# Optimization experiments

Hardware: AMD Instinct MI355X
Metric: run time of the kernel (lower is better)

Reference implementation:

```python
import jax, jax.numpy as jnp
import numpy as np

B, N, E, H = 2, 2048, 2048, 16
D = E // H  # head_dim = 128


def setup_inputs() -> dict:
    key = jax.random.key(0)
    k1, k2, k3, k4 = jax.random.split(key, 4)
    x = jax.random.normal(k1, (B, N, E), dtype=jnp.float32)
    Wq = jax.random.normal(k2, (E, E), dtype=jnp.float32) * 0.02
    Wkv = jax.random.normal(k3, (2 * E, E), dtype=jnp.float32) * 0.02
    Wout = jax.random.normal(k4, (E, E), dtype=jnp.float32) * 0.02
    return {"x": x, "Wq": Wq, "Wkv": Wkv, "Wout": Wout}


def reference(x, Wq, Wkv, Wout):
    # projections (torch Linear: y = x @ W.T)
    q = x @ Wq.T                      # [b, n, e]
    kv = x @ Wkv.T                    # [b, n, 2e]
    k, v = jnp.split(kv, 2, axis=-1)  # each [b, n, e]

    def split_heads(t):
        return t.reshape(B, N, H, D).transpose(0, 2, 1, 3)  # [b, h, n, d]

    q, k, v = split_heads(q), split_heads(k), split_heads(v)

    scale = D ** -0.5
    sim = jnp.einsum('bhid,bhjd->bhij', q * scale, k)  # [b, h, n, n]

    # causal mask: triu(j - i + 1) masks strictly-future positions
    mask_value = -jnp.finfo(sim.dtype).max
    causal_mask = jnp.triu(jnp.ones((N, N), dtype=bool), k=1)
    sim = jnp.where(causal_mask, mask_value, sim)

    attn = jax.nn.softmax(sim, axis=-1)
    out = jnp.einsum('bhij,bhjd->bhid', attn, v)  # [b, h, n, d]
    out = out.transpose(0, 2, 1, 3).reshape(B, N, E)
    return out @ Wout.T
```

## Files before the change

### kernel.cpp

```cpp
#include <hip/hip_runtime.h>


typedef __bf16 bf16;
typedef bf16 bf16x2 __attribute__((ext_vector_type(2)));
typedef bf16 bf16x4 __attribute__((ext_vector_type(4)));
typedef bf16 bf16x8 __attribute__((ext_vector_type(8)));
typedef float f32x4 __attribute__((ext_vector_type(4)));
typedef float f32x16 __attribute__((ext_vector_type(16)));

typedef const __attribute__((address_space(1))) void cg_void;
typedef __attribute__((address_space(3))) void lds_void;

#define MFMA16(a, b, c) __builtin_amdgcn_mfma_f32_16x16x32_bf16((a), (b), (c), 0, 0, 0)
#define MFMA32(a, b, c) __builtin_amdgcn_mfma_f32_32x32x16_bf16((a), (b), (c), 0, 0, 0)

__device__ __forceinline__ void async_load16(const bf16* g, bf16* l) {
  __builtin_amdgcn_global_load_lds((cg_void*)g, (lds_void*)l, 16, 0, 0);
}

__global__ __launch_bounds__(256) void cast_all_kernel(
    const float* __restrict__ x, const float* __restrict__ wq,
    const float* __restrict__ wkv, const float* __restrict__ wout,
    bf16* __restrict__ xb, bf16* __restrict__ wqkvb, bf16* __restrict__ woutb) {
  long i = (long)blockIdx.x * 256 + threadIdx.x;
  const float* src; bf16* dst; long off;
  if (i < 1048576)      { src = x;    dst = xb;            off = i; }
  else if (i < 2621440) { src = wq;   dst = wqkvb;         off = i - 1048576;
                          if (off >= 524288) { src = wkv; dst = wqkvb + 4194304; off -= 524288; } }
  else                  { src = wout; dst = woutb;         off = i - 2621440; }
  float4 f0 = ((const float4*)src)[2 * off];
  float4 f1 = ((const float4*)src)[2 * off + 1];
  bf16x8 o;
  o[0] = (bf16)f0.x; o[1] = (bf16)f0.y; o[2] = (bf16)f0.z; o[3] = (bf16)f0.w;
  o[4] = (bf16)f1.x; o[5] = (bf16)f1.y; o[6] = (bf16)f1.z; o[7] = (bf16)f1.w;
  ((bf16x8*)dst)[off] = o;
}

template <typename OutT>
__global__ __launch_bounds__(256, 4)
void gemm_bt_kernel(const bf16* __restrict__ A, const bf16* __restrict__ B,
                    OutT* __restrict__ C, int K, int NN) {
  __shared__ __attribute__((aligned(16))) bf16 As[128 * 32];
  __shared__ __attribute__((aligned(16))) bf16 Bs[128 * 32];
  const int tid = threadIdx.x;
  const int wave = tid >> 6, lane = tid & 63;
  const int quad = lane >> 4, l15 = lane & 15;
  const int m0 = blockIdx.y * 128, n0 = blockIdx.x * 128;
  const int wm = (wave >> 1) * 64, wn = (wave & 1) * 64;

  f32x4 acc[4][4];
#pragma unroll
  for (int i = 0; i < 4; ++i)
#pragma unroll
    for (int j = 0; j < 4; ++j) acc[i][j] = {0.f, 0.f, 0.f, 0.f};

  const int srow = tid >> 2;
  const int scol = (tid & 3) * 8;
  const bf16* aG = A + (size_t)(m0 + srow) * K + scol;
  const bf16* bG = B + (size_t)(n0 + srow) * K + scol;
  bf16* aL = As + srow * 32 + scol;
  bf16* bL = Bs + srow * 32 + scol;
  const size_t gstep = (size_t)64 * K;

  for (int kt = 0; kt < K; kt += 32) {
    __syncthreads();
    async_load16(aG, aL);
    async_load16(aG + gstep, aL + 64 * 32);
    async_load16(bG, bL);
    async_load16(bG + gstep, bL + 64 * 32);
    aG += 32; bG += 32;
    __syncthreads();

    bf16x8 af[4], bfr[4];
#pragma unroll
    for (int i = 0; i < 4; ++i)
      af[i] = *(const bf16x8*)(As + (wm + i * 16 + l15) * 32 + quad * 8);
#pragma unroll
    for (int j = 0; j < 4; ++j)
      bfr[j] = *(const bf16x8*)(Bs + (wn + j * 16 + l15) * 32 + quad * 8);
#pragma unroll
    for (int i = 0; i < 4; ++i)
#pragma unroll
      for (int j = 0; j < 4; ++j) acc[i][j] = MFMA16(af[i], bfr[j], acc[i][j]);
  }

#pragma unroll
  for (int i = 0; i < 4; ++i) {
#pragma unroll
    for (int r = 0; r < 4; ++r) {
      int row = m0 + wm + i * 16 + quad * 4 + r;
      size_t base = (size_t)row * NN + n0 + wn + l15;
#pragma unroll
      for (int j = 0; j < 4; ++j) C[base + j * 16] = (OutT)acc[i][j][r];
    }
  }
}

__global__ __launch_bounds__(256) void vtrans_kernel(const bf16* __restrict__ qkvb,
                                                     bf16* __restrict__ vt) {
  constexpr int QKV = 6144, NSEQ = 2048, E = 2048;
  __shared__ __attribute__((aligned(16))) bf16 Ts[64 * 64];
  const int t = threadIdx.x;
  const int n0 = blockIdx.x * 64, f0 = blockIdx.y * 64, bb = blockIdx.z;
#pragma unroll
  for (int p = 0; p < 2; ++p) {
    int c = p * 256 + t;
    int i = c >> 3, jc = c & 7;
    bf16x8 v = *(const bf16x8*)(qkvb + (size_t)(bb * NSEQ + n0 + i) * QKV + 4096 + f0 + jc * 8);
    *(bf16x8*)(Ts + i * 64 + ((jc + i) & 7) * 8) = v;
  }
  __syncthreads();
#pragma unroll
  for (int p = 0; p < 2; ++p) {
    int c = p * 256 + t;
    int fl = c >> 3, nl = (c & 7) * 8;
    bf16x8 o;
#pragma unroll
    for (int k = 0; k < 8; ++k) {
      int row = nl + k;
      o[k] = Ts[row * 64 + (((fl >> 3) + row) & 7) * 8 + (fl & 7)];
    }
    *(bf16x8*)(vt + (size_t)(bb * E + f0 + fl) * NSEQ + n0 + nl) = o;
  }
}

__global__ __launch_bounds__(256, 2)
void attn_kernel(const bf16* __restrict__ qkv, const bf16* __restrict__ vt,
                 bf16* __restrict__ yb) {
  constexpr int NSEQ = 2048, E = 2048, QKV = 6144;
  __shared__ __attribute__((aligned(16))) bf16 Ks[2][64 * 128];
  __shared__ __attribute__((aligned(16))) bf16 Vs[2][128 * 64];
  const int tid = threadIdx.x;
  const int wave = tid >> 6, lane = tid & 63;
  const int l31 = lane & 31, half = lane >> 5;
  const int id = blockIdx.x;
  const int slot = (id >> 3) & 15;
  const int bh = (id & 7) | ((id >> 7) << 3);
  const int b = bh >> 4, h = bh & 15;
  const int qt = (slot < 8) ? slot : 23 - slot;
  const float c1 = 0.08838834764831845f * 1.44269504088896f;

  const int krow_s = tid >> 4, kch_s = tid & 15;
  const int vrow_s = tid >> 3, vch_s = tid & 7;
  const bf16* kg = qkv + (size_t)(b * NSEQ) * QKV + 2048 + h * 128;
  const bf16* vg = vt + (size_t)b * E * NSEQ + (size_t)(h * 128) * NSEQ;

  const int diag = 2 * qt + (wave >> 1);
  const int ktmax = 2 * qt + 1;

  {
    bf16* kdst = Ks[0] + tid * 8;
    bf16* vdst = Vs[0] + tid * 8;
#pragma unroll
    for (int p = 0; p < 4; ++p) {
      int r = p * 16 + krow_s;
      async_load16(kg + (size_t)r * QKV + (kch_s ^ (r & 7)) * 8, kdst + p * 2048);
    }
#pragma unroll
    for (int p = 0; p < 4; ++p) {
      int r = p * 32 + vrow_s;
      async_load16(vg + (size_t)r * NSEQ + (vch_s ^ (r & 7)) * 8, vdst + p * 2048);
    }
  }

  const int qrow = qt * 128 + wave * 32 + l31;
  bf16x8 qf[8];
  {
    const bf16* qp = qkv + (size_t)(b * NSEQ + qrow) * QKV + h * 128 + half * 8;
#pragma unroll
    for (int k8 = 0; k8 < 8; ++k8) qf[k8] = *(const bf16x8*)(qp + k8 * 16);
  }

  float m = -3.0e38f, l = 0.f;
  f32x16 accO[4];
#pragma unroll
  for (int md = 0; md < 4; ++md)
#pragma unroll
    for (int r = 0; r < 16; ++r) accO[md][r] = 0.f;

  union PU { unsigned u; bf16x2 h; };
  union FU { bf16x8 v; unsigned u[4]; };

  for (int kt = 0; kt <= ktmax; ++kt) {
    const int cur = kt & 1;
    __syncthreads();

    if (kt < ktmax) {
      const int nxt = kt + 1;
      bf16* kdst = Ks[1 - cur] + tid * 8;
      bf16* vdst = Vs[1 - cur] + tid * 8;
#pragma unroll
      for (int p = 0; p < 4; ++p) {
        int r = p * 16 + krow_s;
        async_load16(kg + (size_t)(nxt * 64 + r) * QKV + (kch_s ^ (r & 7)) * 8, kdst + p * 2048);
      }
#pragma unroll
      for (int p = 0; p < 4; ++p) {
        int r = p * 32 + vrow_s;
        async_load16(vg + (size_t)r * NSEQ + nxt * 64 + (vch_s ^ (r & 7)) * 8, vdst + p * 2048);
      }
    }

    if (kt > diag) continue;

    const bf16* ks = Ks[cur];
    const bf16* vs = Vs[cur];

    f32x16 st[2];
#pragma unroll
    for (int mt = 0; mt < 2; ++mt)
#pragma unroll
      for (int r = 0; r < 16; ++r) st[mt][r] = 0.f;
#pragma unroll
    for (int k8 = 0; k8 < 8; ++k8) {
#pragma unroll
      for (int mt = 0; mt < 2; ++mt) {
        int row = mt * 32 + l31;
        int sl = (k8 * 2 + half) ^ (row & 7);
        bf16x8 kf = *(const bf16x8*)(ks + row * 128 + sl * 8);
        st[mt] = MFMA32(kf, qf[k8], st[mt]);
      }
    }

    if (kt == diag) {
#pragma unroll
      for (int mt = 0; mt < 2; ++mt)
#pragma unroll
        for (int r = 0; r < 16; ++r) {
          int t = kt * 64 + mt * 32 + (r & 3) + 8 * (r >> 2) + 4 * half;
          if (t > qrow) st[mt][r] = -3.0e38f;
        }
    }

    float mx = -3.0e38f;
#pragma unroll
    for (int mt = 0; mt < 2; ++mt)
#pragma unroll
      for (int r = 0; r < 16; ++r) mx = fmaxf(mx, st[mt][r]);
    mx = fmaxf(mx, __shfl_xor(mx, 32));
    float mnew = fmaxf(m, mx);
    float alpha = exp2f((m - mnew) * c1);
    float mc = mnew * c1;
    m = mnew;

    float psum = 0.f;
    unsigned pown[2][4][2];
#pragma unroll
    for (int mt = 0; mt < 2; ++mt)
#pragma unroll
      for (int qd = 0; qd < 4; ++qd)
#pragma unroll
        for (int pr = 0; pr < 2; ++pr) {
          float p0 = exp2f(st[mt][qd * 4 + pr * 2] * c1 - mc);
          float p1 = exp2f(st[mt][qd * 4 + pr * 2 + 1] * c1 - mc);
          psum += p0 + p1;
          PU a; a.h[0] = (bf16)p0; a.h[1] = (bf16)p1;
          pown[mt][qd][pr] = a.u;
        }
    psum += __shfl_xor(psum, 32);
    l = l * alpha + psum;

#pragma unroll
    for (int md = 0; md < 4; ++md)
#pragma unroll
      for (int r = 0; r < 16; ++r) accO[md][r] *= alpha;

#pragma unroll
    for (int mt = 0; mt < 2; ++mt)
#pragma unroll
      for (int c = 0; c < 2; ++c) {
        const int qa = 2 * c, qb = 2 * c + 1;
        unsigned ra0 = __shfl_xor(pown[mt][qa][0], 32);
        unsigned ra1 = __shfl_xor(pown[mt][qa][1], 32);
        unsigned rb0 = __shfl_xor(pown[mt][qb][0], 32);
        unsigned rb1 = __shfl_xor(pown[mt][qb][1], 32);
        FU f;
        f.u[0] = half ? rb0 : pown[mt][qa][0];
        f.u[1] = half ? rb1 : pown[mt][qa][1];
        f.u[2] = half ? pown[mt][qb][0] : ra0;
        f.u[3] = half ? pown[mt][qb][1] : ra1;
        const int kk = mt * 2 + c;
#pragma unroll
        for (int md = 0; md < 4; ++md) {
          int row = md * 32 + l31;
          bf16x8 vf = *(const bf16x8*)(vs + row * 64 + (((kk * 2 + half) ^ (row & 7)) * 8));
          accO[md] = MFMA32(vf, f.v, accO[md]);
        }
      }
  }

  float invl = 1.0f / l;
  bf16* yp = yb + (size_t)(b * NSEQ + qrow) * E + h * 128;
#pragma unroll
  for (int md = 0; md < 4; ++md)
#pragma unroll
    for (int rq = 0; rq < 4; ++rq) {
      bf16x4 o;
#pragma unroll
      for (int i = 0; i < 4; ++i) o[i] = (bf16)(accO[md][rq * 4 + i] * invl);
      *(bf16x4*)(yp + md * 32 + rq * 8 + half * 4) = o;
    }
}

extern "C" void kernel_launch(void* const* d_in, const int* in_sizes, int n_in,
                              void* d_out, int out_size, void* d_ws, size_t ws_size,
                              hipStream_t stream) {
  const float* x    = (const float*)d_in[0];
  const float* Wq   = (const float*)d_in[1];
  const float* Wkv  = (const float*)d_in[2];
  const float* Wout = (const float*)d_in[3];
  float* out = (float*)d_out;

  constexpr size_t NX = (size_t)2 * 2048 * 2048;
  constexpr size_t NW = (size_t)2048 * 2048;

  bf16* xb     = (bf16*)d_ws;
  bf16* wqkvb  = xb + NX;
  bf16* woutb  = wqkvb + 3 * NW;
  bf16* qkv_b  = woutb + NW;
  bf16* y_b    = qkv_b + 3 * NX;
  bf16* vt_b   = xb;

  cast_all_kernel<<<12288, 256, 0, stream>>>(x, Wq, Wkv, Wout, xb, wqkvb, woutb);

  gemm_bt_kernel<bf16><<<dim3(48, 32), 256, 0, stream>>>(xb, wqkvb, qkv_b, 2048, 6144);
  vtrans_kernel<<<dim3(32, 32, 2), 256, 0, stream>>>(qkv_b, vt_b);
  attn_kernel<<<512, 256, 0, stream>>>(qkv_b, vt_b, y_b);
  gemm_bt_kernel<float><<<dim3(16, 32), 256, 0, stream>>>(y_b, woutb, out, 2048, 2048);
}
```

Measured before the change: 396.8 us.

## Fuse V transpose into QKV GEMM epilogue and drop separate transpose kernel

The QKV projection GEMM now writes Q and K to a narrower buffer, while tiles in the V column range are transposed through shared memory and written directly in V^T layout. This removes the standalone transpose kernel, its launch, and the extra read and write of V. The attention kernel is adapted to the new Q/K row stride, and its block-to-(batch, head, query tile) mapping is reordered. The cost is two extra block barriers and a scalar LDS gather in the epilogue of the V tiles.

```diff
diff --git a/kernel.cpp b/kernel.cpp
--- a/kernel.cpp
+++ b/kernel.cpp
@@ -36,12 +36,13 @@
   ((bf16x8*)dst)[off] = o;
 }
 
-template <typename OutT>
+template <typename OutT, bool SPLITV>
 __global__ __launch_bounds__(256, 4)
 void gemm_bt_kernel(const bf16* __restrict__ A, const bf16* __restrict__ B,
-                    OutT* __restrict__ C, int K, int NN) {
-  __shared__ __attribute__((aligned(16))) bf16 As[128 * 32];
-  __shared__ __attribute__((aligned(16))) bf16 Bs[128 * 32];
+                    OutT* __restrict__ C, int K, int NN, bf16* __restrict__ vt) {
+  __shared__ __attribute__((aligned(16))) bf16 smem[8192];
+  bf16* As = smem;
+  bf16* Bs = smem + 4096;
   const int tid = threadIdx.x;
   const int wave = tid >> 6, lane = tid & 63;
   const int quad = lane >> 4, l15 = lane & 15;
@@ -84,6 +85,43 @@
       for (int j = 0; j < 4; ++j) acc[i][j] = MFMA16(af[i], bfr[j], acc[i][j]);
   }
 
+  if (SPLITV && n0 >= 4096) {
+    const int f0 = n0 - 4096;
+    const int b = m0 >> 11;
+    const int nbase = m0 & 2047;
+#pragma unroll
+    for (int p = 0; p < 2; ++p) {
+      __syncthreads();
+      if ((wave >> 1) == p) {
+#pragma unroll
+        for (int i = 0; i < 4; ++i)
+#pragma unroll
+          for (int r = 0; r < 4; ++r) {
+            int nl = i * 16 + quad * 4 + r;
+#pragma unroll
+            for (int j = 0; j < 4; ++j) {
+              int f = wn + j * 16 + l15;
+              smem[nl * 128 + ((((f >> 3) + nl) & 15) * 8) + (f & 7)] = (bf16)acc[i][j][r];
+            }
+          }
+      }
+      __syncthreads();
+#pragma unroll
+      for (int c = 0; c < 4; ++c) {
+        int idx = c * 256 + tid;
+        int f = idx >> 3, n8 = idx & 7;
+        bf16x8 o;
+#pragma unroll
+        for (int k = 0; k < 8; ++k) {
+          int nl = n8 * 8 + k;
+          o[k] = smem[nl * 128 + ((((f >> 3) + nl) & 15) * 8) + (f & 7)];
+        }
+        *(bf16x8*)(vt + ((size_t)(b * 2048 + f0 + f)) * 2048 + nbase + p * 64 + n8 * 8) = o;
+      }
+    }
+    return;
+  }
+
 #pragma unroll
   for (int i = 0; i < 4; ++i) {
 #pragma unroll
@@ -96,53 +134,25 @@
   }
 }
 
-__global__ __launch_bounds__(256) void vtrans_kernel(const bf16* __restrict__ qkvb,
-                                                     bf16* __restrict__ vt) {
-  constexpr int QKV = 6144, NSEQ = 2048, E = 2048;
-  __shared__ __attribute__((aligned(16))) bf16 Ts[64 * 64];
-  const int t = threadIdx.x;
-  const int n0 = blockIdx.x * 64, f0 = blockIdx.y * 64, bb = blockIdx.z;
-#pragma unroll
-  for (int p = 0; p < 2; ++p) {
-    int c = p * 256 + t;
-    int i = c >> 3, jc = c & 7;
-    bf16x8 v = *(const bf16x8*)(qkvb + (size_t)(bb * NSEQ + n0 + i) * QKV + 4096 + f0 + jc * 8);
-    *(bf16x8*)(Ts + i * 64 + ((jc + i) & 7) * 8) = v;
-  }
-  __syncthreads();
-#pragma unroll
-  for (int p = 0; p < 2; ++p) {
-    int c = p * 256 + t;
-    int fl = c >> 3, nl = (c & 7) * 8;
-    bf16x8 o;
-#pragma unroll
-    for (int k = 0; k < 8; ++k) {
-      int row = nl + k;
-      o[k] = Ts[row * 64 + (((fl >> 3) + row) & 7) * 8 + (fl & 7)];
-    }
-    *(bf16x8*)(vt + (size_t)(bb * E + f0 + fl) * NSEQ + n0 + nl) = o;
-  }
-}
-
 __global__ __launch_bounds__(256, 2)
-void attn_kernel(const bf16* __restrict__ qkv, const bf16* __restrict__ vt,
+void attn_kernel(const bf16* __restrict__ qk, const bf16* __restrict__ vt,
                  bf16* __restrict__ yb) {
-  constexpr int NSEQ = 2048, E = 2048, QKV = 6144;
+  constexpr int NSEQ = 2048, E = 2048, QKS = 4096;
   __shared__ __attribute__((aligned(16))) bf16 Ks[2][64 * 128];
   __shared__ __attribute__((aligned(16))) bf16 Vs[2][128 * 64];
   const int tid = threadIdx.x;
   const int wave = tid >> 6, lane = tid & 63;
   const int l31 = lane & 31, half = lane >> 5;
   const int id = blockIdx.x;
-  const int slot = (id >> 3) & 15;
-  const int bh = (id & 7) | ((id >> 7) << 3);
+  const int slot = (id >> 5) & 15;
+  const int bh = (id & 7) | (((id >> 3) & 3) << 3);
   const int b = bh >> 4, h = bh & 15;
   const int qt = (slot < 8) ? slot : 23 - slot;
   const float c1 = 0.08838834764831845f * 1.44269504088896f;
 
   const int krow_s = tid >> 4, kch_s = tid & 15;
   const int vrow_s = tid >> 3, vch_s = tid & 7;
-  const bf16* kg = qkv + (size_t)(b * NSEQ) * QKV + 2048 + h * 128;
+  const bf16* kg = qk + (size_t)(b * NSEQ) * QKS + 2048 + h * 128;
   const bf16* vg = vt + (size_t)b * E * NSEQ + (size_t)(h * 128) * NSEQ;
 
   const int diag = 2 * qt + (wave >> 1);
@@ -154,7 +164,7 @@
 #pragma unroll
     for (int p = 0; p < 4; ++p) {
       int r = p * 16 + krow_s;
-      async_load16(kg + (size_t)r * QKV + (kch_s ^ (r & 7)) * 8, kdst + p * 2048);
+      async_load16(kg + (size_t)r * QKS + (kch_s ^ (r & 7)) * 8, kdst + p * 2048);
     }
 #pragma unroll
     for (int p = 0; p < 4; ++p) {
@@ -166,7 +176,7 @@
   const int qrow = qt * 128 + wave * 32 + l31;
   bf16x8 qf[8];
   {
-    const bf16* qp = qkv + (size_t)(b * NSEQ + qrow) * QKV + h * 128 + half * 8;
+    const bf16* qp = qk + (size_t)(b * NSEQ + qrow) * QKS + h * 128 + half * 8;
 #pragma unroll
     for (int k8 = 0; k8 < 8; ++k8) qf[k8] = *(const bf16x8*)(qp + k8 * 16);
   }
@@ -192,7 +202,7 @@
 #pragma unroll
       for (int p = 0; p < 4; ++p) {
         int r = p * 16 + krow_s;
-        async_load16(kg + (size_t)(nxt * 64 + r) * QKV + (kch_s ^ (r & 7)) * 8, kdst + p * 2048);
+        async_load16(kg + (size_t)(nxt * 64 + r) * QKS + (kch_s ^ (r & 7)) * 8, kdst + p * 2048);
       }
 #pragma unroll
       for (int p = 0; p < 4; ++p) {
@@ -317,14 +327,15 @@
   bf16* xb     = (bf16*)d_ws;
   bf16* wqkvb  = xb + NX;
   bf16* woutb  = wqkvb + 3 * NW;
-  bf16* qkv_b  = woutb + NW;
-  bf16* y_b    = qkv_b + 3 * NX;
-  bf16* vt_b   = xb;
+  bf16* qk_b   = woutb + NW;
+  bf16* y_b    = qk_b + 2 * NX;
+  bf16* vt_b   = y_b + NX;
 
   cast_all_kernel<<<12288, 256, 0, stream>>>(x, Wq, Wkv, Wout, xb, wqkvb, woutb);
 
-  gemm_bt_kernel<bf16><<<dim3(48, 32), 256, 0, stream>>>(xb, wqkvb, qkv_b, 2048, 6144);
-  vtrans_kernel<<<dim3(32, 32, 2), 256, 0, stream>>>(qkv_b, vt_b);
-  attn_kernel<<<512, 256, 0, stream>>>(qkv_b, vt_b, y_b);
-  gemm_bt_kernel<float><<<dim3(16, 32), 256, 0, stream>>>(y_b, woutb, out, 2048, 2048);
-}
+  gemm_bt_kernel<bf16, true><<<dim3(48, 32), 256, 0, stream>>>(
+      xb, wqkvb, qk_b, 2048, 4096, vt_b);
+  attn_kernel<<<512, 256, 0, stream>>>(qk_b, vt_b, y_b);
+  gemm_bt_kernel<float, false><<<dim3(16, 32), 256, 0, stream>>>(
+      y_b, woutb, out, 2048, 2048, nullptr);
+}
```

Result: faster. 383.3 us (-3.4%).
